# Optimization experiments

Hardware: AMD Instinct MI355X
Metric: run time of the kernel (lower is better)

## Reference

```python
import jax, jax.numpy as jnp
import numpy as np
from jax import lax


def _compute_Bp(lam):
    # Bʹ[k, j] = 1 / prod_{i != j} (1 - λ_i / λ_j), via log-sum for stability.
    k, n = lam.shape
    ratios = lam[:, :, None] / lam[:, None, :]           # [k, n, n], entry (i, j) = λ_i / λ_j
    eye = jnp.eye(n, dtype=bool)[None]                    # zero out diagonal (log(1-0)=0)
    ratios = jnp.where(eye, jnp.zeros((), ratios.dtype), ratios)
    lnBp = -jnp.sum(jnp.log(1.0 - ratios), axis=1)        # [k, n]
    return jnp.exp(lnBp)


def _linear_recurrence(a, b):
    # s_t = a_t * s_{t-1} + b_t (elementwise, diagonal), parallel associative scan over time.
    def combine(c1, c2):
        a1, b1 = c1
        a2, b2 = c2
        return a1 * a2, b1 * a2 + b2
    return lax.associative_scan(combine, (a, b), axis=0)[1]


def _ldstack_forward(x, R, theta, lnC_r, lnC_i, D, Do):
    b, T, d = x.shape
    k, half_n = theta.shape
    n = 2 * half_n
    m = D.shape[1]

    # average=True path: project d -> k, go time-major, lift to complex
    xp = jnp.einsum('btd,dk->btk', x, R)
    xc = jnp.transpose(xp, (1, 0, 2)).astype(jnp.complex64)      # [T, b, k]

    # unitary_constitute: λ = exp(i * [θ, -θ]) on the unit circle
    lam = jnp.exp(jnp.concatenate([theta, -theta], axis=1) * 1j)  # [k, n] complex64
    Cp = jnp.exp(lnC_r + 1j * lnC_i)                              # [k, n, m] complex64

    Bp = _compute_Bp(lam)                                         # [k, n]
    Bx = xc[..., None] * Bp                                       # [T, b, k, n]
    al = jnp.broadcast_to(lam, (T, b, k, n))                      # α is None for Δ=1

    # standard=True: shift coefficients one step (state lags input)
    zeros = jnp.zeros((1, b, k, n), dtype=jnp.complex64)
    al = jnp.concatenate([zeros, al[:-1]], axis=0)
    Bx = jnp.concatenate([zeros, Bx[:-1]], axis=0)

    s = _linear_recurrence(al, Bx)                                # [T, b, k, n]

    Cs = jnp.einsum('tbkn,knm->tbkm', s, Cp)                      # readout
    Dx = xc[..., None] * D.astype(jnp.complex64)[None, None]      # [T, b, k, m]
    y = Cs + Dx + Do.astype(jnp.complex64)                        # [T, b, k, m]

    y = jnp.mean(y, axis=2)                                       # average over k
    y = jnp.real(y)                                               # [T, b, m]
    return jnp.transpose(y, (1, 0, 2))                            # [b, T, m]


def setup_inputs() -> dict:
    b, T, d = 8, 2048, 128
    k, n, m = 32, 32, 128
    key = jax.random.key(0)
    ks = jax.random.split(key, 7)
    x = jax.random.normal(ks[0], (b, T, d), dtype=jnp.float32)
    R = jax.random.normal(ks[1], (d, k), dtype=jnp.float32)
    theta = jax.random.uniform(ks[2], (k, n // 2), dtype=jnp.float32,
                               minval=-np.pi, maxval=np.pi)
    lnC_r = 1e-4 * jax.random.normal(ks[3], (k, n, m), dtype=jnp.float32)
    lnC_i = 1e-4 * jax.random.normal(ks[4], (k, n, m), dtype=jnp.float32)
    D = jax.random.uniform(ks[5], (k, m), dtype=jnp.float32, minval=-1e-3, maxval=1e-3)
    Do = jax.random.uniform(ks[6], (m,), dtype=jnp.float32, minval=-1e-7, maxval=1e-7)
    return {"x": x, "R": R, "theta": theta, "lnC_r": lnC_r, "lnC_i": lnC_i,
            "D": D, "Do": Do}


def reference(x, R, theta, lnC_r, lnC_i, D, Do):
    return _ldstack_forward(x, R, theta, lnC_r, lnC_i, D, Do)
```

## Files before the change

### kernel.cpp

```cpp
#include <hip/hip_runtime.h>
#include <hip/hip_bf16.h>
#include <math.h>

#define K_  32
#define HN  16
#define N_  32
#define M_  128
#define B_  8
#define T_  2048
#define D_  128
#define BT  (B_*T_)
#define KA  1056
#define CHK 32
#define CL  64

typedef short short8 __attribute__((ext_vector_type(8)));
typedef float floatx4 __attribute__((ext_vector_type(4)));
typedef unsigned short ushort_t;
typedef unsigned int uint_t;

__device__ __forceinline__ ushort_t f2bf(float f) {
    __hip_bfloat16 h = __float2bfloat16(f);
    return *reinterpret_cast<ushort_t*>(&h);
}
__device__ __forceinline__ uint_t pack_bf2(float re, float im) {
    return ((uint_t)f2bf(im) << 16) | (uint_t)f2bf(re);
}

__global__ __launch_bounds__(256) void k_pre(const float* __restrict__ theta,
                                             const float* __restrict__ lnC_r,
                                             const float* __restrict__ lnC_i,
                                             const float* __restrict__ D,
                                             const float* __restrict__ x,
                                             const float* __restrict__ R,
                                             float* __restrict__ ws,
                                             ushort_t* __restrict__ Wt,
                                             float* __restrict__ xpT,
                                             ushort_t* __restrict__ A2) {
    __shared__ float xls[32 * 128];
    int bid = blockIdx.x, tid = threadIdx.x;
    if (bid == 0) {
        #pragma unroll
        for (int rep = 0; rep < 2; ++rep) {
            int t2 = rep * 256 + tid;
            int k = t2 >> 4, j = t2 & 15;
            float angj = theta[k * HN + j];
            float pr = 1.f, pi = 0.f;
            for (int i = 0; i < N_; ++i) {
                if (i == j) continue;
                float angi = (i < HN) ? theta[k * HN + i] : -theta[k * HN + i - HN];
                float d = angi - angj;
                float tr = 1.f - cosf(d);
                float ti = -sinf(d);
                float nr = pr * tr - pi * ti;
                float ni = pr * ti + pi * tr;
                pr = nr; pi = ni;
            }
            float den = pr * pr + pi * pi;
            ws[t2]        = cosf(angj);
            ws[512 + t2]  = sinf(angj);
            ws[1024 + t2] = pr / den;
            ws[1536 + t2] = -pi / den;
        }
    } else if (bid <= 272) {
        int t = (bid - 1) * 256 + tid;
        const float inv = 1.f / 32.f;
        if (t < K_ * HN * M_) {
            int m = t & 127, j = (t >> 7) & 15, k = t >> 11;
            int i0 = (k * N_ + j) * M_ + m;
            int i1 = (k * N_ + j + HN) * M_ + m;
            float r0 = expf(lnC_r[i0]), c0 = cosf(lnC_i[i0]), s0 = sinf(lnC_i[i0]);
            float r1 = expf(lnC_r[i1]), c1 = cosf(lnC_i[i1]), s1 = sinf(lnC_i[i1]);
            float wr = (r0 * c0 + r1 * c1) * inv;
            float wi = (r1 * s1 - r0 * s0) * inv;
            *(uint_t*)(Wt + (size_t)m * KA + k * 32 + 2 * j) = pack_bf2(wr, wi);
        } else if (t < K_ * HN * M_ + K_ * M_) {
            int u = t - K_ * HN * M_;
            int m = u & 127, k = u >> 7;
            Wt[(size_t)m * KA + 1024 + k] = f2bf(D[k * M_ + m] * inv);
        }
    } else {
        int xb = bid - 273;
        int b = xb >> 6;
        int tbase = (xb & 63) * 32;
        const float4* xsrc = (const float4*)(x + ((size_t)b * T_ + tbase) * D_);
        float4* xd = (float4*)xls;
        #pragma unroll
        for (int e = 0; e < 4; ++e) xd[tid + 256 * e] = xsrc[tid + 256 * e];
        __syncthreads();
        int kk = tid & 31, rg = tid >> 5;
        float accv[4] = {0.f, 0.f, 0.f, 0.f};
        #pragma unroll 4
        for (int i = 0; i < D_; ++i) {
            float rv = R[i * K_ + kk];
            #pragma unroll
            for (int rr = 0; rr < 4; ++rr)
                accv[rr] += xls[(rg + 8 * rr) * D_ + i] * rv;
        }
        #pragma unroll
        for (int rr = 0; rr < 4; ++rr) {
            int tt = tbase + rg + 8 * rr;
            A2[(size_t)(tt * 8 + b) * KA + 1024 + kk] = f2bf(accv[rr]);
            size_t base = (size_t)(b * K_ + kk) * T_;
            if (tt < T_ - 1) xpT[base + tt + 1] = accv[rr];
            if (tt == 0)     xpT[base] = 0.f;
        }
    }
}

__global__ __launch_bounds__(512) void k_scan(const float* __restrict__ xpT,
                                              const float* __restrict__ ws,
                                              uint_t* __restrict__ A2u) {
    __shared__ float xls[T_];
    __shared__ float Er[512], Ei[512];

    int tid = threadIdx.x;
    int k = blockIdx.x & 31, b = blockIdx.x >> 5;
    int c = tid >> 4, j = tid & 15;
    int col = k * 16 + j;

    ((float4*)xls)[tid] = ((const float4*)(xpT + (size_t)(b * K_ + k) * T_))[tid];
    __syncthreads();

    float lr = ws[col], li = ws[512 + col];
    float br = ws[1024 + col], bi = ws[1536 + col];

    {
        float sr = 0.f, si = 0.f;
        const float* xc = xls + c * CL;
        #pragma unroll 4
        for (int p = 0; p < CL; ++p) {
            float x1 = xc[p];
            float nr = br * x1 + lr * sr - li * si;
            float ni = bi * x1 + lr * si + li * sr;
            sr = nr; si = ni;
        }
        Er[c * 16 + j] = sr;
        Ei[c * 16 + j] = si;
    }
    __syncthreads();

    if (tid < 16) {
        float pr = lr, pi = li;
        #pragma unroll
        for (int q = 0; q < 6; ++q) {
            float nr = pr * pr - pi * pi;
            float ni = 2.f * pr * pi;
            pr = nr; pi = ni;
        }
        float sr = 0.f, si = 0.f;
        for (int cc = 0; cc < CHK; ++cc) {
            int idx = cc * 16 + tid;
            float er = Er[idx], ei = Ei[idx];
            Er[idx] = sr; Ei[idx] = si;
            float nr = pr * sr - pi * si + er;
            float ni = pr * si + pi * sr + ei;
            sr = nr; si = ni;
        }
    }
    __syncthreads();

    {
        float sr = Er[c * 16 + j], si = Ei[c * 16 + j];
        int t0 = c * CL;
        const float* xc = xls + t0;
        uint_t* Ab = A2u + (size_t)(t0 * 8 + b) * (KA / 2) + col;
        #pragma unroll 4
        for (int p = 0; p < CL; ++p) {
            float x1 = xc[p];
            float nr = br * x1 + lr * sr - li * si;
            float ni = bi * x1 + lr * si + li * sr;
            sr = nr; si = ni;
            Ab[0] = pack_bf2(sr, si);
            Ab += 8 * (KA / 2);
        }
    }
}

__global__ __launch_bounds__(256, 2) void k_gemm(const ushort_t* __restrict__ A2,
                                                 const ushort_t* __restrict__ Wt,
                                                 const float* __restrict__ Do,
                                                 float* __restrict__ out) {
    int tid = threadIdx.x;
    int wave = tid >> 6;
    int rh = wave & 1;
    int chh = wave >> 1;
    int lane = tid & 63;
    int l16 = lane & 15;
    int quad = lane >> 4;
    int row0 = blockIdx.x * 32 + rh * 16;

    const ushort_t* Ap = A2 + (size_t)(row0 + l16) * KA + quad * 8;
    const ushort_t* Wp = Wt + (size_t)(chh * 64 + l16) * KA + quad * 8;

    floatx4 acc[4];
    #pragma unroll
    for (int n = 0; n < 4; ++n) acc[n] = (floatx4){0.f, 0.f, 0.f, 0.f};

    for (int g = 0; g < 11; ++g) {
        int k0 = g * 96;
        short8 a0 = *(const short8*)(Ap + k0);
        short8 a1 = *(const short8*)(Ap + k0 + 32);
        short8 a2 = *(const short8*)(Ap + k0 + 64);
        short8 bv[4][3];
        #pragma unroll
        for (int n = 0; n < 4; ++n) {
            #pragma unroll
            for (int s = 0; s < 3; ++s)
                bv[n][s] = *(const short8*)(Wp + (size_t)n * 16 * KA + k0 + s * 32);
        }
        #pragma unroll
        for (int n = 0; n < 4; ++n)
            acc[n] = __builtin_amdgcn_mfma_f32_16x16x32_bf16(a0, bv[n][0], acc[n], 0, 0, 0);
        #pragma unroll
        for (int n = 0; n < 4; ++n)
            acc[n] = __builtin_amdgcn_mfma_f32_16x16x32_bf16(a1, bv[n][1], acc[n], 0, 0, 0);
        #pragma unroll
        for (int n = 0; n < 4; ++n)
            acc[n] = __builtin_amdgcn_mfma_f32_16x16x32_bf16(a2, bv[n][2], acc[n], 0, 0, 0);
    }

    #pragma unroll
    for (int n = 0; n < 4; ++n) {
        int col = chh * 64 + n * 16 + l16;
        float dov = Do[col];
        #pragma unroll
        for (int q = 0; q < 4; ++q) {
            int r = row0 + quad * 4 + q;
            int b = r & 7, t = r >> 3;
            out[(size_t)(b * T_ + t) * M_ + col] = acc[n][q] + dov;
        }
    }
}

extern "C" void kernel_launch(void* const* d_in, const int* in_sizes, int n_in,
                              void* d_out, int out_size, void* d_ws, size_t ws_size,
                              hipStream_t stream) {
    const float* x     = (const float*)d_in[0];
    const float* R     = (const float*)d_in[1];
    const float* theta = (const float*)d_in[2];
    const float* lnC_r = (const float*)d_in[3];
    const float* lnC_i = (const float*)d_in[4];
    const float* D     = (const float*)d_in[5];
    const float* Do    = (const float*)d_in[6];
    float* out = (float*)d_out;

    float* wsf   = (float*)d_ws;
    float* lambp = wsf;
    ushort_t* Wt = (ushort_t*)(wsf + 2048);
    ushort_t* A2 = (ushort_t*)(wsf + 2048 + 67584);
    float* xpT   = wsf + 2048 + 67584 + 8650752;

    k_pre<<<785, 256, 0, stream>>>(theta, lnC_r, lnC_i, D, x, R,
                                   lambp, Wt, xpT, A2);
    k_scan<<<256, 512, 0, stream>>>(xpT, lambp, (uint_t*)A2);
    k_gemm<<<512, 256, 0, stream>>>(A2, Wt, Do, out);
}
```

Measured before the change: 128.2 us.

## Stage A tile in swizzled LDS and split GEMM columns across eight waves

The GEMM kernel now copies each block's 32-row A tile into shared memory with an XOR swizzle, so it is read from global memory once instead of by two waves per row half. The block grows to 512 threads, and each of the eight waves computes two 16-column output tiles instead of four, which spreads the MFMA work across more waves. This costs a full-tile load and a barrier before compute, and leaves less unrolled load-compute overlap per wave. Global W reads now come from a smaller set of columns per wave.

Measured after the change: 126.9 us. No clear change (-1.0%).

```diff
diff --git a/kernel.cpp b/kernel.cpp
--- a/kernel.cpp
+++ b/kernel.cpp
@@ -13,6 +13,7 @@
 #define KA  1056
 #define CHK 32
 #define CL  64
+#define ABYTES 2176
 
 typedef short short8 __attribute__((ext_vector_type(8)));
 typedef float floatx4 __attribute__((ext_vector_type(4)));
@@ -177,59 +178,52 @@
     }
 }
 
-__global__ __launch_bounds__(256, 2) void k_gemm(const ushort_t* __restrict__ A2,
-                                                 const ushort_t* __restrict__ Wt,
-                                                 const float* __restrict__ Do,
-                                                 float* __restrict__ out) {
+__global__ __launch_bounds__(512) void k_gemm2(const uint_t* __restrict__ A2u,
+                                               const ushort_t* __restrict__ Wt,
+                                               const float* __restrict__ Do,
+                                               float* __restrict__ out) {
+    __shared__ __align__(16) char smem[32 * ABYTES];
+
     int tid = threadIdx.x;
-    int wave = tid >> 6;
-    int rh = wave & 1;
-    int chh = wave >> 1;
-    int lane = tid & 63;
-    int l16 = lane & 15;
-    int quad = lane >> 4;
-    int row0 = blockIdx.x * 32 + rh * 16;
-
-    const ushort_t* Ap = A2 + (size_t)(row0 + l16) * KA + quad * 8;
-    const ushort_t* Wp = Wt + (size_t)(chh * 64 + l16) * KA + quad * 8;
-
-    floatx4 acc[4];
+    int bid = blockIdx.x;
+
+    const uint_t* src = A2u + (size_t)bid * (32 * (KA / 2));
+    for (int it = 0; it < 33; ++it) {
+        int f = it * 512 + tid;
+        int row = f / 528;
+        int uc = f - row * 528;
+        int bo = (row * ABYTES + uc * 4) ^ ((row & 7) << 4);
+        *(uint_t*)(smem + bo) = src[f];
+    }
+    __syncthreads();
+
+    int wave = tid >> 6, lane = tid & 63;
+    int l16 = lane & 15, quad = lane >> 4;
+    int rh = wave & 1, cf = wave >> 1;
+    int arow = rh * 16 + l16;
+    int abase = arow * ABYTES + quad * 16;
+    int aswz = (arow & 7) << 4;
+    const ushort_t* Wp0 = Wt + (size_t)(cf * 32 + l16) * KA + quad * 8;
+    const ushort_t* Wp1 = Wp0 + (size_t)16 * KA;
+
+    floatx4 acc0 = {0.f, 0.f, 0.f, 0.f}, acc1 = {0.f, 0.f, 0.f, 0.f};
+    for (int ks = 0; ks < 33; ++ks) {
+        short8 av = *(const short8*)(smem + ((abase + ks * 64) ^ aswz));
+        short8 b0 = *(const short8*)(Wp0 + ks * 32);
+        short8 b1 = *(const short8*)(Wp1 + ks * 32);
+        acc0 = __builtin_amdgcn_mfma_f32_16x16x32_bf16(av, b0, acc0, 0, 0, 0);
+        acc1 = __builtin_amdgcn_mfma_f32_16x16x32_bf16(av, b1, acc1, 0, 0, 0);
+    }
+
+    int col0 = cf * 32 + l16;
+    float dv0 = Do[col0], dv1 = Do[col0 + 16];
     #pragma unroll
-    for (int n = 0; n < 4; ++n) acc[n] = (floatx4){0.f, 0.f, 0.f, 0.f};
-
-    for (int g = 0; g < 11; ++g) {
-        int k0 = g * 96;
-        short8 a0 = *(const short8*)(Ap + k0);
-        short8 a1 = *(const short8*)(Ap + k0 + 32);
-        short8 a2 = *(const short8*)(Ap + k0 + 64);
-        short8 bv[4][3];
-        #pragma unroll
-        for (int n = 0; n < 4; ++n) {
-            #pragma unroll
-            for (int s = 0; s < 3; ++s)
-                bv[n][s] = *(const short8*)(Wp + (size_t)n * 16 * KA + k0 + s * 32);
-        }
-        #pragma unroll
-        for (int n = 0; n < 4; ++n)
-            acc[n] = __builtin_amdgcn_mfma_f32_16x16x32_bf16(a0, bv[n][0], acc[n], 0, 0, 0);
-        #pragma unroll
-        for (int n = 0; n < 4; ++n)
-            acc[n] = __builtin_amdgcn_mfma_f32_16x16x32_bf16(a1, bv[n][1], acc[n], 0, 0, 0);
-        #pragma unroll
-        for (int n = 0; n < 4; ++n)
-            acc[n] = __builtin_amdgcn_mfma_f32_16x16x32_bf16(a2, bv[n][2], acc[n], 0, 0, 0);
-    }
-
-    #pragma unroll
-    for (int n = 0; n < 4; ++n) {
-        int col = chh * 64 + n * 16 + l16;
-        float dov = Do[col];
-        #pragma unroll
-        for (int q = 0; q < 4; ++q) {
-            int r = row0 + quad * 4 + q;
-            int b = r & 7, t = r >> 3;
-            out[(size_t)(b * T_ + t) * M_ + col] = acc[n][q] + dov;
-        }
+    for (int q = 0; q < 4; ++q) {
+        int r = bid * 32 + rh * 16 + quad * 4 + q;
+        int b = r & 7, t = r >> 3;
+        float* op = out + (size_t)(b * T_ + t) * M_;
+        op[col0]      = acc0[q] + dv0;
+        op[col0 + 16] = acc1[q] + dv1;
     }
 }
 
@@ -254,5 +248,5 @@
     k_pre<<<785, 256, 0, stream>>>(theta, lnC_r, lnC_i, D, x, R,
                                    lambp, Wt, xpT, A2);
     k_scan<<<256, 512, 0, stream>>>(xpT, lambp, (uint_t*)A2);
-    k_gemm<<<512, 256, 0, stream>>>(A2, Wt, Do, out);
-}
+    k_gemm2<<<512, 512, 0, stream>>>((const uint_t*)A2, Wt, Do, out);
+}
```
